# Kernel tuning notes

Measured on AMD Instinct MI355X. Metric: run time of the kernel, lower is better.

## Reference

```python
import jax, jax.numpy as jnp
import numpy as np

D_MODEL = 1024
NHEAD = 16
D_FF = 4 * D_MODEL
EPS = 1e-5


def layer_norm(x, gamma, beta):
    mu = jnp.mean(x, axis=-1, keepdims=True)
    var = jnp.mean(jnp.square(x - mu), axis=-1, keepdims=True)
    return (x - mu) * jax.lax.rsqrt(var + EPS) * gamma + beta


def setup_inputs() -> dict:
    key = jax.random.key(0)
    ks = jax.random.split(key, 12)
    B, S, D = 4, 2048, D_MODEL
    s = 1.0 / np.sqrt(D)
    return {
        "x": jax.random.normal(ks[0], (B, S, D), jnp.float32),
        "wq": jax.random.normal(ks[1], (D, D), jnp.float32) * s,
        "wk": jax.random.normal(ks[2], (D, D), jnp.float32) * s,
        "wv": jax.random.normal(ks[3], (D, D), jnp.float32) * s,
        "wo": jax.random.normal(ks[4], (D, D), jnp.float32) * s,
        "bo": jnp.zeros((D,), jnp.float32),
        "ln1_g": jnp.ones((D,), jnp.float32),
        "ln1_b": jnp.zeros((D,), jnp.float32),
        "ln2_g": jnp.ones((D,), jnp.float32),
        "ln2_b": jnp.zeros((D,), jnp.float32),
        "w1": jax.random.normal(ks[5], (D, D_FF), jnp.float32) * s,
        "b1": jnp.zeros((D_FF,), jnp.float32),
        "w2": jax.random.normal(ks[6], (D_FF, D), jnp.float32) * (1.0 / np.sqrt(D_FF)),
        "b2": jnp.zeros((D,), jnp.float32),
    }


def reference(x, wq, wk, wv, wo, bo, ln1_g, ln1_b, ln2_g, ln2_b, w1, b1, w2, b2):
    B, S, D = x.shape
    H = NHEAD
    Dh = D // H
    xn = layer_norm(x, ln1_g, ln1_b)
    # projections -> [B, H, S, Dh]
    q = jnp.einsum('bsd,de->bse', xn, wq).reshape(B, S, H, Dh).transpose(0, 2, 1, 3)
    k = jnp.einsum('bsd,de->bse', xn, wk).reshape(B, S, H, Dh).transpose(0, 2, 1, 3)
    v = jnp.einsum('bsd,de->bse', xn, wv).reshape(B, S, H, Dh).transpose(0, 2, 1, 3)
    scores = jnp.einsum('bhsd,bhtd->bhst', q, k) / np.sqrt(Dh)  # [B,H,S,S]
    attn = jax.nn.softmax(scores, axis=-1)
    ctx = jnp.einsum('bhst,bhtd->bhsd', attn, v)
    ctx = ctx.transpose(0, 2, 1, 3).reshape(B, S, D)
    att_out = jnp.einsum('bsd,de->bse', ctx, wo) + bo
    xt = x + att_out
    h = layer_norm(xt, ln2_g, ln2_b)
    ffn = jnp.einsum('bsf,fd->bsd', jax.nn.relu(jnp.einsum('bsd,df->bsf', h, w1) + b1), w2) + b2
    return xt + ffn
```

## Files before the change

### kernel.cpp

```cpp
#include <hip/hip_runtime.h>
#include <stdint.h>

typedef __attribute__((ext_vector_type(8))) __bf16 bf16x8;
typedef __attribute__((ext_vector_type(4))) float f32x4;
typedef unsigned short u16;

#define D_MODEL 1024
#define D_FF 4096
#define SEQ 2048
#define NHEAD 16
#define DH 64
#define MROWS 8192
#define LDST 72

__device__ __forceinline__ u16 f2bf(float f) {
  union { float f; unsigned u; } v; v.f = f;
  unsigned r = v.u + 0x7fffu + ((v.u >> 16) & 1u);
  return (u16)(r >> 16);
}

__device__ __forceinline__ void gload16(const u16* g, u16* l) {
  __builtin_amdgcn_global_load_lds((const __attribute__((address_space(1))) void*)(g),
                                   (__attribute__((address_space(3))) void*)(l),
                                   16, 0, 0);
}

__device__ __forceinline__ void block_bar() {
  asm volatile("" ::: "memory");
  __builtin_amdgcn_s_barrier();
  asm volatile("" ::: "memory");
}

template <int N>
__device__ __forceinline__ void wait_vm() {
  if constexpr (N == 6)      asm volatile("s_waitcnt vmcnt(6)" ::: "memory");
  else if constexpr (N == 4) asm volatile("s_waitcnt vmcnt(4)" ::: "memory");
  else                       asm volatile("s_waitcnt vmcnt(0)" ::: "memory");
}

__global__ __launch_bounds__(256)
void wconv_kernel(const float* __restrict__ W, u16* __restrict__ Wt, int K, int N,
                  float scale) {
  __shared__ u16 t[32][33];
  const int tid = threadIdx.x, tx = tid & 31, ty = tid >> 5;
  const int n0 = blockIdx.x * 32, k0 = blockIdx.y * 32;
#pragma unroll
  for (int i = 0; i < 4; ++i) {
    int k = ty + i * 8;
    t[k][tx] = f2bf(W[(size_t)(k0 + k) * N + n0 + tx] * scale);
  }
  __syncthreads();
#pragma unroll
  for (int i = 0; i < 4; ++i) {
    int n = ty + i * 8;
    Wt[(size_t)(n0 + n) * K + k0 + tx] = t[tx][n];
  }
}

__global__ __launch_bounds__(256)
void ln_kernel(const float* __restrict__ x, u16* __restrict__ out,
               const float* __restrict__ g, const float* __restrict__ beta) {
  const int row = blockIdx.x, tid = threadIdx.x;
  const float4 v = reinterpret_cast<const float4*>(x + (size_t)row * D_MODEL)[tid];
  float s = v.x + v.y + v.z + v.w;
#pragma unroll
  for (int off = 32; off; off >>= 1) s += __shfl_down(s, off);
  __shared__ float red[8];
  if ((tid & 63) == 0) red[tid >> 6] = s;
  __syncthreads();
  const float mu = (red[0] + red[1] + red[2] + red[3]) * (1.0f / D_MODEL);
  const float dx = v.x - mu, dy = v.y - mu, dz = v.z - mu, dw = v.w - mu;
  float sq = dx * dx + dy * dy + dz * dz + dw * dw;
#pragma unroll
  for (int off = 32; off; off >>= 1) sq += __shfl_down(sq, off);
  if ((tid & 63) == 0) red[4 + (tid >> 6)] = sq;
  __syncthreads();
  const float var = (red[4] + red[5] + red[6] + red[7]) * (1.0f / D_MODEL);
  const float rs = rsqrtf(var + 1e-5f);
  const float4 gv = reinterpret_cast<const float4*>(g)[tid];
  const float4 bv = reinterpret_cast<const float4*>(beta)[tid];
  ushort4 ov;
  ov.x = f2bf(dx * rs * gv.x + bv.x);
  ov.y = f2bf(dy * rs * gv.y + bv.y);
  ov.z = f2bf(dz * rs * gv.z + bv.z);
  ov.w = f2bf(dw * rs * gv.w + bv.w);
  reinterpret_cast<ushort4*>(out + (size_t)row * D_MODEL)[tid] = ov;
}

template <int BM, int EPI>
__global__ __launch_bounds__(512, 2)
void gemm8p_kernel(const u16* __restrict__ A, const u16* __restrict__ Bt,
                   int N, int K,
                   const float* __restrict__ bias,
                   const float* __restrict__ res,
                   float* __restrict__ outf, u16* __restrict__ outb,
                   u16* __restrict__ outb2, u16* __restrict__ outb3) {
  constexpr int WM = BM / 2;
  constexpr int MREP = WM / 16;
  constexpr int MI = MREP / 4;
  constexpr int ACH = BM / 64;
  constexpr int VN = (BM == 256) ? 6 : 4;
  __shared__ __align__(16) u16 Al[2][BM * 64];
  __shared__ __align__(16) u16 Bl[2][256 * 64];
  const int tid = threadIdx.x, lane = tid & 63, wave = tid >> 6;
  const int wr = wave >> 2, wc = wave & 3;
  const int l16 = lane & 15, g8 = lane >> 4;
  const int srw = lane >> 3;
  const int scl = ((lane & 7) ^ (lane >> 3)) * 8;
  const int swz = (l16 & 7) << 3;
  const int mBase = blockIdx.y * BM, nBase = blockIdx.x * 256;
  const int nt = K >> 6;

  f32x4 acc[MREP][4];
#pragma unroll
  for (int mi = 0; mi < MREP; ++mi)
#pragma unroll
    for (int nj = 0; nj < 4; ++nj) acc[mi][nj] = f32x4{0.f, 0.f, 0.f, 0.f};

  auto stageChunk = [&](int tile, int c) {
    if (tile >= nt) return;
    const int buf = tile & 1;
    if (c < ACH) {
      const int r0 = c * 64 + wave * 8;
      gload16(A + (size_t)(mBase + r0 + srw) * K + tile * 64 + scl,
              &Al[buf][r0 * 64]);
    } else {
      const int r0 = (c - ACH) * 64 + wave * 8;
      gload16(Bt + (size_t)(nBase + r0 + srw) * K + tile * 64 + scl,
              &Bl[buf][r0 * 64]);
    }
  };

  constexpr int STO256[16] = {1,1, 2,2, 2,2, 2,2, 2,2, 3,3, 3,3, 3,3};
  constexpr int STC256[16] = {1,3, 4,5, 6,7, 0,2, 1,3, 4,5, 6,7, 0,2};
  constexpr int STO128[16] = {1,1, 2,2, 2,2, 0,0, 2,2, 3,3, 3,3, 0,0};
  constexpr int STC128[16] = {0,1, 2,3, 4,5, -1,-1, 0,1, 2,3, 4,5, -1,-1};

  constexpr int P0_256[8] = {4,5,6,7,0,2,1,3};
  constexpr int P1_256[6] = {4,5,6,7,0,2};
  constexpr int P0_128[6] = {2,3,4,5,0,1};
  constexpr int P1_128[4] = {2,3,4,5};
  if constexpr (BM == 256) {
#pragma unroll
    for (int i = 0; i < 8; ++i) stageChunk(0, P0_256[i]);
#pragma unroll
    for (int i = 0; i < 6; ++i) stageChunk(1, P1_256[i]);
  } else {
#pragma unroll
    for (int i = 0; i < 6; ++i) stageChunk(0, P0_128[i]);
#pragma unroll
    for (int i = 0; i < 4; ++i) stageChunk(1, P1_128[i]);
  }
  wait_vm<VN>();
  block_bar();

  for (int T = 0; T < nt; T += 2) {
    bf16x8 bfr[4][2];
#pragma unroll
    for (int p = 0; p < 8; ++p) {
      const int q = p & 3;
      const int buf = p >> 2;
      if (q == 0) {
#pragma unroll
        for (int nj = 0; nj < 4; ++nj)
#pragma unroll
          for (int ks = 0; ks < 2; ++ks) {
            const int rb = wc * 64 + nj * 16 + l16;
            bfr[nj][ks] = *reinterpret_cast<const bf16x8*>(
                &Bl[buf][rb * 64 + ((ks * 32 + g8 * 8) ^ swz)]);
          }
      }
      bf16x8 af[MI][2];
#pragma unroll
      for (int i = 0; i < MI; ++i)
#pragma unroll
        for (int ks = 0; ks < 2; ++ks) {
          const int ra = wr * WM + (q * MI + i) * 16 + l16;
          af[i][ks] = *reinterpret_cast<const bf16x8*>(
              &Al[buf][ra * 64 + ((ks * 32 + g8 * 8) ^ swz)]);
        }
      if constexpr (BM == 256) {
        stageChunk(T + STO256[2 * p], STC256[2 * p]);
        stageChunk(T + STO256[2 * p + 1], STC256[2 * p + 1]);
      } else {
        if (STC128[2 * p] >= 0) {
          stageChunk(T + STO128[2 * p], STC128[2 * p]);
          stageChunk(T + STO128[2 * p + 1], STC128[2 * p + 1]);
        }
      }
      block_bar();
      __builtin_amdgcn_s_setprio(1);
#pragma unroll
      for (int i = 0; i < MI; ++i)
#pragma unroll
        for (int nj = 0; nj < 4; ++nj)
#pragma unroll
          for (int ks = 0; ks < 2; ++ks)
            acc[q * MI + i][nj] = __builtin_amdgcn_mfma_f32_16x16x32_bf16(
                af[i][ks], bfr[nj][ks], acc[q * MI + i][nj], 0, 0, 0);
      __builtin_amdgcn_s_setprio(0);
      if (p == 3) {
        if (T + 2 < nt) wait_vm<VN>(); else wait_vm<0>();
      } else if (p == 7) {
        wait_vm<VN>();
      }
      block_bar();
    }
  }

#pragma unroll
  for (int mi = 0; mi < MREP; ++mi)
#pragma unroll
    for (int nj = 0; nj < 4; ++nj) {
      const int colB = wc * 64 + nj * 16 + l16;
      const int row0 = mBase + wr * WM + mi * 16 + g8 * 4;
      if (EPI == 4) {
        const int seg = nBase >> 10;
        const int c = (nBase & 1023) + colB;
        if (seg == 2) {
          const int bi = row0 >> 11, s = row0 & 2047;
          ushort4 pk;
          pk.x = f2bf(acc[mi][nj][0]);
          pk.y = f2bf(acc[mi][nj][1]);
          pk.z = f2bf(acc[mi][nj][2]);
          pk.w = f2bf(acc[mi][nj][3]);
          *reinterpret_cast<ushort4*>(outb3 + ((size_t)(bi << 10) + c) * SEQ + s) = pk;
        } else {
          u16* o = (seg == 0) ? outb : outb2;
#pragma unroll
          for (int r = 0; r < 4; ++r)
            o[(size_t)(row0 + r) * D_MODEL + c] = f2bf(acc[mi][nj][r]);
        }
      } else {
        const int col = nBase + colB;
        const float bv = bias[col];
#pragma unroll
        for (int r = 0; r < 4; ++r) {
          const size_t idx = (size_t)(row0 + r) * N + col;
          const float vv = acc[mi][nj][r];
          if (EPI == 1) {
            outf[idx] = vv + bv + res[idx];
          } else {
            const float tv = vv + bv;
            outb[idx] = f2bf(tv > 0.f ? tv : 0.f);
          }
        }
      }
    }
}

__global__ __launch_bounds__(256)
void attn_kernel(const u16* __restrict__ qb, const u16* __restrict__ kb,
                 const u16* __restrict__ vb, u16* __restrict__ ctx) {
  __shared__ u16 Kl[64 * LDST];
  __shared__ u16 Vl[64 * LDST];
  __shared__ u16 Pl[4][32 * LDST];
  const int tid = threadIdx.x;
  const int lane = tid & 63, wave = tid >> 6, g8 = lane >> 4, l16 = lane & 15;
  const int b = blockIdx.y >> 4, h = blockIdx.y & 15;
  const int q0 = blockIdx.x * 128 + wave * 32;
  const size_t rowB = (size_t)b * SEQ;
  const int colH = h * DH;
  const size_t vtBase = (size_t)(b * 1024 + colH) * SEQ;

  bf16x8 qf[2][2];
#pragma unroll
  for (int m = 0; m < 2; ++m)
#pragma unroll
    for (int ks = 0; ks < 2; ++ks)
      qf[m][ks] = *reinterpret_cast<const bf16x8*>(
          qb + (rowB + q0 + m * 16 + l16) * D_MODEL + colH + ks * 32 + g8 * 8);

  float mi[2] = {-1e30f, -1e30f}, li[2] = {0.f, 0.f};
  f32x4 o[2][4];
#pragma unroll
  for (int m = 0; m < 2; ++m)
#pragma unroll
    for (int nt = 0; nt < 4; ++nt) o[m][nt] = f32x4{0.f, 0.f, 0.f, 0.f};

  const int srow = tid >> 3, scol = (tid & 7) * 8;

  for (int t0 = 0; t0 < SEQ; t0 += 64) {
#pragma unroll
    for (int i = 0; i < 2; ++i) {
      const int row = srow + i * 32;
      *reinterpret_cast<int4*>(&Kl[row * LDST + scol]) =
          *reinterpret_cast<const int4*>(kb + (rowB + t0 + row) * D_MODEL + colH + scol);
      *reinterpret_cast<int4*>(&Vl[row * LDST + scol]) =
          *reinterpret_cast<const int4*>(vb + vtBase + (size_t)row * SEQ + t0 + scol);
    }
    __syncthreads();

    f32x4 st[2][4];
#pragma unroll
    for (int m = 0; m < 2; ++m)
#pragma unroll
      for (int kt = 0; kt < 4; ++kt) st[m][kt] = f32x4{0.f, 0.f, 0.f, 0.f};
#pragma unroll
    for (int kt = 0; kt < 4; ++kt) {
      const bf16x8 kf0 = *reinterpret_cast<const bf16x8*>(&Kl[(kt * 16 + l16) * LDST + g8 * 8]);
      const bf16x8 kf1 = *reinterpret_cast<const bf16x8*>(&Kl[(kt * 16 + l16) * LDST + 32 + g8 * 8]);
#pragma unroll
      for (int m = 0; m < 2; ++m) {
        st[m][kt] = __builtin_amdgcn_mfma_f32_16x16x32_bf16(kf0, qf[m][0], st[m][kt], 0, 0, 0);
        st[m][kt] = __builtin_amdgcn_mfma_f32_16x16x32_bf16(kf1, qf[m][1], st[m][kt], 0, 0, 0);
      }
    }

    float alpha[2];
#pragma unroll
    for (int m = 0; m < 2; ++m) {
      float pmax = st[m][0][0];
#pragma unroll
      for (int kt = 0; kt < 4; ++kt)
#pragma unroll
        for (int r = 0; r < 4; ++r) pmax = fmaxf(pmax, st[m][kt][r]);
      pmax = fmaxf(pmax, __shfl_xor(pmax, 16));
      pmax = fmaxf(pmax, __shfl_xor(pmax, 32));
      const float mnew = fmaxf(mi[m], pmax);
      alpha[m] = __expf(mi[m] - mnew);
      mi[m] = mnew;
      float sum = 0.f;
#pragma unroll
      for (int kt = 0; kt < 4; ++kt) {
        ushort4 pk;
#pragma unroll
        for (int r = 0; r < 4; ++r) {
          const float p = __expf(st[m][kt][r] - mnew);
          sum += p;
          ((u16*)&pk)[r] = f2bf(p);
        }
        *reinterpret_cast<ushort4*>(&Pl[wave][(m * 16 + l16) * LDST + kt * 16 + g8 * 4]) = pk;
      }
      sum += __shfl_xor(sum, 16);
      sum += __shfl_xor(sum, 32);
      li[m] = li[m] * alpha[m] + sum;
    }

#pragma unroll
    for (int m = 0; m < 2; ++m) {
      f32x4 al;
#pragma unroll
      for (int r = 0; r < 4; ++r) al[r] = __shfl(alpha[m], g8 * 4 + r);
#pragma unroll
      for (int nt = 0; nt < 4; ++nt) {
        f32x4 t = o[m][nt];
        t[0] *= al[0]; t[1] *= al[1]; t[2] *= al[2]; t[3] *= al[3];
        o[m][nt] = t;
      }
    }

    bf16x8 pf[2][2];
#pragma unroll
    for (int m = 0; m < 2; ++m)
#pragma unroll
      for (int ks = 0; ks < 2; ++ks)
        pf[m][ks] = *reinterpret_cast<const bf16x8*>(&Pl[wave][(m * 16 + l16) * LDST + ks * 32 + g8 * 8]);
#pragma unroll
    for (int nt = 0; nt < 4; ++nt) {
      const bf16x8 vf0 = *reinterpret_cast<const bf16x8*>(&Vl[(nt * 16 + l16) * LDST + g8 * 8]);
      const bf16x8 vf1 = *reinterpret_cast<const bf16x8*>(&Vl[(nt * 16 + l16) * LDST + 32 + g8 * 8]);
#pragma unroll
      for (int m = 0; m < 2; ++m) {
        o[m][nt] = __builtin_amdgcn_mfma_f32_16x16x32_bf16(pf[m][0], vf0, o[m][nt], 0, 0, 0);
        o[m][nt] = __builtin_amdgcn_mfma_f32_16x16x32_bf16(pf[m][1], vf1, o[m][nt], 0, 0, 0);
      }
    }
    __syncthreads();
  }

#pragma unroll
  for (int m = 0; m < 2; ++m) {
    f32x4 ld;
#pragma unroll
    for (int r = 0; r < 4; ++r) ld[r] = 1.0f / __shfl(li[m], g8 * 4 + r);
#pragma unroll
    for (int nt = 0; nt < 4; ++nt)
#pragma unroll
      for (int r = 0; r < 4; ++r) {
        const float v = o[m][nt][r] * ld[r];
        ctx[(rowB + q0 + m * 16 + g8 * 4 + r) * D_MODEL + colH + nt * 16 + l16] = f2bf(v);
      }
  }
}

extern "C" void kernel_launch(void* const* d_in, const int* in_sizes, int n_in,
                              void* d_out, int out_size, void* d_ws, size_t ws_size,
                              hipStream_t stream) {
  const float* x   = (const float*)d_in[0];
  const float* wq  = (const float*)d_in[1];
  const float* wk  = (const float*)d_in[2];
  const float* wv  = (const float*)d_in[3];
  const float* wo  = (const float*)d_in[4];
  const float* bo  = (const float*)d_in[5];
  const float* l1g = (const float*)d_in[6];
  const float* l1b = (const float*)d_in[7];
  const float* l2g = (const float*)d_in[8];
  const float* l2b = (const float*)d_in[9];
  const float* w1  = (const float*)d_in[10];
  const float* b1  = (const float*)d_in[11];
  const float* w2  = (const float*)d_in[12];
  const float* b2  = (const float*)d_in[13];
  float* outp = (float*)d_out;

  uint8_t* ws = (uint8_t*)d_ws;
  const size_t MB = 1024 * 1024;
  u16* wqkvt = (u16*)(ws + 0 * MB);
  u16* wqt   = wqkvt;
  u16* wkt   = (u16*)(ws + 2 * MB);
  u16* wvt   = (u16*)(ws + 4 * MB);
  u16* wot   = (u16*)(ws + 6 * MB);
  u16* w1t   = (u16*)(ws + 8 * MB);
  u16* w2t   = (u16*)(ws + 16 * MB);
  u16* xn    = (u16*)(ws + 24 * MB);
  u16* qbuf  = (u16*)(ws + 40 * MB);
  u16* kbuf  = (u16*)(ws + 56 * MB);
  u16* vbufT = (u16*)(ws + 72 * MB);
  u16* ctx   = xn;
  u16* hbuf  = qbuf;
  u16* ffh   = kbuf;

  dim3 blk(256);
  dim3 blk5(512);

  wconv_kernel<<<dim3(32, 32), blk, 0, stream>>>(wq, wqt, 1024, 1024, 0.125f);
  wconv_kernel<<<dim3(32, 32), blk, 0, stream>>>(wk, wkt, 1024, 1024, 1.0f);
  wconv_kernel<<<dim3(32, 32), blk, 0, stream>>>(wv, wvt, 1024, 1024, 1.0f);
  wconv_kernel<<<dim3(32, 32), blk, 0, stream>>>(wo, wot, 1024, 1024, 1.0f);
  wconv_kernel<<<dim3(128, 32), blk, 0, stream>>>(w1, w1t, 1024, 4096, 1.0f);
  wconv_kernel<<<dim3(32, 128), blk, 0, stream>>>(w2, w2t, 4096, 1024, 1.0f);

  ln_kernel<<<MROWS, blk, 0, stream>>>(x, xn, l1g, l1b);

  gemm8p_kernel<128, 4><<<dim3(12, 64), blk5, 0, stream>>>(
      xn, wqkvt, 3072, 1024, nullptr, nullptr, nullptr, qbuf, kbuf, vbufT);

  attn_kernel<<<dim3(16, 64), blk, 0, stream>>>(qbuf, kbuf, vbufT, ctx);

  gemm8p_kernel<128, 1><<<dim3(4, 64), blk5, 0, stream>>>(
      ctx, wot, 1024, 1024, bo, x, outp, nullptr, nullptr, nullptr);

  ln_kernel<<<MROWS, blk, 0, stream>>>(outp, hbuf, l2g, l2b);

  gemm8p_kernel<256, 2><<<dim3(16, 32), blk5, 0, stream>>>(
      hbuf, w1t, 4096, 1024, b1, nullptr, nullptr, ffh, nullptr, nullptr);

  gemm8p_kernel<128, 1><<<dim3(4, 64), blk5, 0, stream>>>(
      ffh, w2t, 1024, 4096, b2, outp, outp, nullptr, nullptr, nullptr);
}
```

Baseline: 603.5 us.

## Double-buffer attention K/V tiles with async LDS loads, XOR swizzle, exp2 softmax

The attention kernel now stages K and V tiles with global_load_lds into double-buffered shared memory, so the load of the next tile is issued before the current tile is computed. Padded LDS rows are replaced with an XOR swizzle to avoid bank conflicts. Softmax switches to native exp2, with log2(e) folded into the Q weight scale. Float-to-bf16 conversion now uses the hardware cast instead of manual rounding. This doubles the K/V LDS footprint and relies on the swizzle being consistent across writers and readers.

```diff
diff --git a/kernel.cpp b/kernel.cpp
--- a/kernel.cpp
+++ b/kernel.cpp
@@ -2,6 +2,7 @@
 #include <stdint.h>
 
 typedef __attribute__((ext_vector_type(8))) __bf16 bf16x8;
+typedef __attribute__((ext_vector_type(4))) __bf16 bf16x4;
 typedef __attribute__((ext_vector_type(4))) float f32x4;
 typedef unsigned short u16;
 
@@ -11,7 +12,6 @@
 #define NHEAD 16
 #define DH 64
 #define MROWS 8192
-#define LDST 72
 
 __device__ __forceinline__ u16 f2bf(float f) {
   union { float f; unsigned u; } v; v.f = f;
@@ -252,9 +252,9 @@
 __global__ __launch_bounds__(256)
 void attn_kernel(const u16* __restrict__ qb, const u16* __restrict__ kb,
                  const u16* __restrict__ vb, u16* __restrict__ ctx) {
-  __shared__ u16 Kl[64 * LDST];
-  __shared__ u16 Vl[64 * LDST];
-  __shared__ u16 Pl[4][32 * LDST];
+  __shared__ __align__(16) u16 Kl[2][64 * 64];
+  __shared__ __align__(16) u16 Vl[2][64 * 64];
+  __shared__ __align__(16) u16 Pl[4][32 * 64];
   const int tid = threadIdx.x;
   const int lane = tid & 63, wave = tid >> 6, g8 = lane >> 4, l16 = lane & 15;
   const int b = blockIdx.y >> 4, h = blockIdx.y & 15;
@@ -262,6 +262,9 @@
   const size_t rowB = (size_t)b * SEQ;
   const int colH = h * DH;
   const size_t vtBase = (size_t)(b * 1024 + colH) * SEQ;
+  const int srw = lane >> 3;
+  const int scl = ((lane & 7) ^ (lane >> 3)) * 8;
+  const int cswz = (l16 & 7) * 8;
 
   bf16x8 qf[2][2];
 #pragma unroll
@@ -278,18 +281,23 @@
 #pragma unroll
     for (int nt = 0; nt < 4; ++nt) o[m][nt] = f32x4{0.f, 0.f, 0.f, 0.f};
 
-  const int srow = tid >> 3, scol = (tid & 7) * 8;
-
-  for (int t0 = 0; t0 < SEQ; t0 += 64) {
+  auto stageKV = [&](int t0, int buf) {
+    if (t0 >= SEQ) return;
 #pragma unroll
     for (int i = 0; i < 2; ++i) {
-      const int row = srow + i * 32;
-      *reinterpret_cast<int4*>(&Kl[row * LDST + scol]) =
-          *reinterpret_cast<const int4*>(kb + (rowB + t0 + row) * D_MODEL + colH + scol);
-      *reinterpret_cast<int4*>(&Vl[row * LDST + scol]) =
-          *reinterpret_cast<const int4*>(vb + vtBase + (size_t)row * SEQ + t0 + scol);
-    }
-    __syncthreads();
+      const int r0 = wave * 16 + i * 8;
+      gload16(kb + (rowB + t0 + r0 + srw) * D_MODEL + colH + scl, &Kl[buf][r0 * 64]);
+      gload16(vb + vtBase + (size_t)(r0 + srw) * SEQ + t0 + scl, &Vl[buf][r0 * 64]);
+    }
+  };
+
+  stageKV(0, 0);
+  wait_vm<0>();
+  block_bar();
+
+  int buf = 0;
+  for (int t0 = 0; t0 < SEQ; t0 += 64, buf ^= 1) {
+    stageKV(t0 + 64, buf ^ 1);
 
     f32x4 st[2][4];
 #pragma unroll
@@ -298,8 +306,10 @@
       for (int kt = 0; kt < 4; ++kt) st[m][kt] = f32x4{0.f, 0.f, 0.f, 0.f};
 #pragma unroll
     for (int kt = 0; kt < 4; ++kt) {
-      const bf16x8 kf0 = *reinterpret_cast<const bf16x8*>(&Kl[(kt * 16 + l16) * LDST + g8 * 8]);
-      const bf16x8 kf1 = *reinterpret_cast<const bf16x8*>(&Kl[(kt * 16 + l16) * LDST + 32 + g8 * 8]);
+      const bf16x8 kf0 = *reinterpret_cast<const bf16x8*>(
+          &Kl[buf][(kt * 16 + l16) * 64 + ((g8 * 8) ^ cswz)]);
+      const bf16x8 kf1 = *reinterpret_cast<const bf16x8*>(
+          &Kl[buf][(kt * 16 + l16) * 64 + ((32 + g8 * 8) ^ cswz)]);
 #pragma unroll
       for (int m = 0; m < 2; ++m) {
         st[m][kt] = __builtin_amdgcn_mfma_f32_16x16x32_bf16(kf0, qf[m][0], st[m][kt], 0, 0, 0);
@@ -318,19 +328,21 @@
       pmax = fmaxf(pmax, __shfl_xor(pmax, 16));
       pmax = fmaxf(pmax, __shfl_xor(pmax, 32));
       const float mnew = fmaxf(mi[m], pmax);
-      alpha[m] = __expf(mi[m] - mnew);
+      alpha[m] = __builtin_amdgcn_exp2f(mi[m] - mnew);
       mi[m] = mnew;
       float sum = 0.f;
 #pragma unroll
       for (int kt = 0; kt < 4; ++kt) {
-        ushort4 pk;
+        bf16x4 pk;
 #pragma unroll
         for (int r = 0; r < 4; ++r) {
-          const float p = __expf(st[m][kt][r] - mnew);
+          const float p = __builtin_amdgcn_exp2f(st[m][kt][r] - mnew);
           sum += p;
-          ((u16*)&pk)[r] = f2bf(p);
+          pk[r] = (__bf16)p;
         }
-        *reinterpret_cast<ushort4*>(&Pl[wave][(m * 16 + l16) * LDST + kt * 16 + g8 * 4]) = pk;
+        const int row = m * 16 + l16;
+        *reinterpret_cast<bf16x4*>(
+            &Pl[wave][row * 64 + ((kt * 16 + g8 * 4) ^ cswz)]) = pk;
       }
       sum += __shfl_xor(sum, 16);
       sum += __shfl_xor(sum, 32);
@@ -355,18 +367,23 @@
     for (int m = 0; m < 2; ++m)
 #pragma unroll
       for (int ks = 0; ks < 2; ++ks)
-        pf[m][ks] = *reinterpret_cast<const bf16x8*>(&Pl[wave][(m * 16 + l16) * LDST + ks * 32 + g8 * 8]);
+        pf[m][ks] = *reinterpret_cast<const bf16x8*>(
+            &Pl[wave][(m * 16 + l16) * 64 + ((ks * 32 + g8 * 8) ^ cswz)]);
 #pragma unroll
     for (int nt = 0; nt < 4; ++nt) {
-      const bf16x8 vf0 = *reinterpret_cast<const bf16x8*>(&Vl[(nt * 16 + l16) * LDST + g8 * 8]);
-      const bf16x8 vf1 = *reinterpret_cast<const bf16x8*>(&Vl[(nt * 16 + l16) * LDST + 32 + g8 * 8]);
+      const bf16x8 vf0 = *reinterpret_cast<const bf16x8*>(
+          &Vl[buf][(nt * 16 + l16) * 64 + ((g8 * 8) ^ cswz)]);
+      const bf16x8 vf1 = *reinterpret_cast<const bf16x8*>(
+          &Vl[buf][(nt * 16 + l16) * 64 + ((32 + g8 * 8) ^ cswz)]);
 #pragma unroll
       for (int m = 0; m < 2; ++m) {
         o[m][nt] = __builtin_amdgcn_mfma_f32_16x16x32_bf16(pf[m][0], vf0, o[m][nt], 0, 0, 0);
         o[m][nt] = __builtin_amdgcn_mfma_f32_16x16x32_bf16(pf[m][1], vf1, o[m][nt], 0, 0, 0);
       }
     }
-    __syncthreads();
+
+    wait_vm<0>();
+    block_bar();
   }
 
 #pragma unroll
@@ -378,8 +395,9 @@
     for (int nt = 0; nt < 4; ++nt)
 #pragma unroll
       for (int r = 0; r < 4; ++r) {
-        const float v = o[m][nt][r] * ld[r];
-        ctx[(rowB + q0 + m * 16 + g8 * 4 + r) * D_MODEL + colH + nt * 16 + l16] = f2bf(v);
+        const __bf16 v = (__bf16)(o[m][nt][r] * ld[r]);
+        ctx[(rowB + q0 + m * 16 + g8 * 4 + r) * D_MODEL + colH + nt * 16 + l16] =
+            __builtin_bit_cast(u16, v);
       }
   }
 }
@@ -423,7 +441,7 @@
   dim3 blk(256);
   dim3 blk5(512);
 
-  wconv_kernel<<<dim3(32, 32), blk, 0, stream>>>(wq, wqt, 1024, 1024, 0.125f);
+  wconv_kernel<<<dim3(32, 32), blk, 0, stream>>>(wq, wqt, 1024, 1024, 0.18033688011112042f);
   wconv_kernel<<<dim3(32, 32), blk, 0, stream>>>(wk, wkt, 1024, 1024, 1.0f);
   wconv_kernel<<<dim3(32, 32), blk, 0, stream>>>(wv, wvt, 1024, 1024, 1.0f);
   wconv_kernel<<<dim3(32, 32), blk, 0, stream>>>(wo, wot, 1024, 1024, 1.0f);
```

Measured after the change: 553.2 us. 8.3% less time.
